# Kernel optimization log

Measured on AMD Instinct MI355X. Metric: run time of the kernel, lower is better.

## Reference

```python
import jax, jax.numpy as jnp
import numpy as np

B, T, C = 8, 2048, 1024      # batch, timesteps, input_dim
G, E = 2, 320                # groups_dim, entries_dim
EMB = 512                    # emb_dim
D = EMB // G                 # true_emb_dim per group


def setup_inputs() -> dict:
    key = jax.random.key(0)
    k1, k2, k3 = jax.random.split(key, 3)
    X = jax.random.normal(k1, (B, T, C), dtype=jnp.float32)
    # nn.Linear(input_dim, G*E): weight (out,in) ~ N(0,1), bias zeros
    W = jax.random.normal(k2, (G * E, C), dtype=jnp.float32)
    b = jnp.zeros((G * E,), dtype=jnp.float32)
    # codebook Parameter(1, G*E, D) ~ U[0,1); stored squeezed as (G*E, D)
    codebook = jax.random.uniform(k3, (G * E, D), dtype=jnp.float32)
    return {"X": X, "W": W, "b": b, "codebook": codebook}


def reference(X, W, b, codebook):
    # Eval-mode forward of VectorQuantization (time_first=True).
    nB, nT, _ = X.shape
    logits = jnp.einsum("btc,kc->btk", X, W) + b           # (B, T, G*E)
    # Faithful to source: view (B,T,G*E) as (B*G, T*E) and argmax over last dim
    flat = logits.reshape(nB * G, nT * E)                   # (B*G, T*E)
    k = jnp.argmax(flat, axis=-1)                           # (B*G,)
    hard = jax.nn.one_hot(k, nT * E, dtype=logits.dtype)    # (B*G, T*E)
    q = hard.reshape(nB * nT, G, E)                         # (B*T, G, E)
    # (one-hot * codebook).sum over entries == per-group gather
    cb = codebook.reshape(G, E, D)                          # (G, E, D)
    out = jnp.einsum("nge,ged->ngd", q, cb)                 # (B*T, G, D)
    return out.reshape(nB, nT, G * D)                       # (B, T, emb_dim)
```

## Files before the change

### kernel.cpp

```cpp
#include <hip/hip_runtime.h>
#include <stdint.h>

#define CC    1024
#define EE    320
#define KN    640
#define DD    256
#define MTOT  16384
#define NBLK  640
#define OUT4  2097152
#define MARGIN 12.0f

typedef __attribute__((ext_vector_type(8))) short short8;
typedef __attribute__((ext_vector_type(4))) float f32x4;
typedef __attribute__((ext_vector_type(2))) long longx2;

__device__ __forceinline__ unsigned int f32_orderable(float x) {
    unsigned int b = __float_as_uint(x);
    return (b & 0x80000000u) ? ~b : (b | 0x80000000u);
}

__global__ void init_slots_kernel(unsigned long long* __restrict__ slots) {
    if (threadIdx.x < 17) slots[threadIdx.x] = 0ull;
}

__global__ __launch_bounds__(256)
void convert_kernel(const float* __restrict__ X, const float* __restrict__ W,
                    unsigned char* __restrict__ A2F8, unsigned char* __restrict__ B2F8,
                    unsigned long long* __restrict__ slots, float* __restrict__ out) {
    const int bid = blockIdx.x;
    const int tid = threadIdx.x;
    {
        f32x4 z = {0.f, 0.f, 0.f, 0.f};
#pragma unroll
        for (int j = 0; j < 2; j++) {
            int zidx = bid * 512 + j * 256 + tid;
            if (zidx < OUT4) __builtin_nontemporal_store(z, (f32x4*)out + zidx);
        }
    }
    const int lane = tid & 63;
    const float* src;
    unsigned char* dst;
    int punit;
    if (bid < 4096) {
        punit = bid * 4 + (tid >> 6);
        src = X; dst = A2F8;
    } else {
        if (bid == 4096 && tid < 17) slots[tid] = 0ull;
        punit = (bid - 4096) * 4 + (tid >> 6);
        src = W; dst = B2F8;
    }
    int rt = punit >> 4, kc2 = punit & 15;
    int row = rt * 16 + (lane & 15);
    int col = kc2 * 64 + ((lane >> 4) << 3);
    const float* p = src + (size_t)row * CC + col;
    float4 v0 = *(const float4*)p;
    float4 v1 = *(const float4*)(p + 4);
    float4 v2 = *(const float4*)(p + 32);
    float4 v3 = *(const float4*)(p + 36);
    int d0 = __builtin_amdgcn_cvt_pk_fp8_f32(v0.x, v0.y, 0, false);
    d0     = __builtin_amdgcn_cvt_pk_fp8_f32(v0.z, v0.w, d0, true);
    int d1 = __builtin_amdgcn_cvt_pk_fp8_f32(v1.x, v1.y, 0, false);
    d1     = __builtin_amdgcn_cvt_pk_fp8_f32(v1.z, v1.w, d1, true);
    int d2 = __builtin_amdgcn_cvt_pk_fp8_f32(v2.x, v2.y, 0, false);
    d2     = __builtin_amdgcn_cvt_pk_fp8_f32(v2.z, v2.w, d2, true);
    int d3 = __builtin_amdgcn_cvt_pk_fp8_f32(v3.x, v3.y, 0, false);
    d3     = __builtin_amdgcn_cvt_pk_fp8_f32(v3.z, v3.w, d3, true);
    *(int4*)(dst + (size_t)punit * 1024 + lane * 16) = make_int4(d0, d1, d2, d3);
}

__global__ __launch_bounds__(256, 3)
void gemm_argmax_mfma(const unsigned char* __restrict__ A2F8,
                      const unsigned char* __restrict__ B2F8,
                      const float* __restrict__ X,
                      const float* __restrict__ W,
                      const float* __restrict__ bias,
                      const float* __restrict__ codebook,
                      float* __restrict__ out,
                      unsigned long long* __restrict__ slots,
                      unsigned int* __restrict__ counter) {
    __shared__ float redf[4];
    __shared__ int cnt_s;
    __shared__ int cand_s[128];
    __shared__ unsigned int done_s;
    __shared__ unsigned long long s16[16];

    const int tid  = threadIdx.x;
    const int lane = tid & 63;
    const int wave = tid >> 6;

    const int l   = blockIdx.x;
    const int xcd = l & 7;
    const int w   = l >> 3;
    const int mt  = xcd * 16 + w / 5;
    const int nt  = w % 5;
    const int m0 = mt * 128;
    const int n0 = nt * 128;

    const int wm = (wave >> 1) * 64;
    const int wn = (wave & 1) * 64;

    const unsigned char* Ap[4];
    const unsigned char* Bp[4];
#pragma unroll
    for (int t = 0; t < 4; t++) {
        Ap[t] = A2F8 + ((size_t)(((m0 + wm) >> 4) + t) * 16) * 1024 + lane * 16;
        Bp[t] = B2F8 + ((size_t)(((n0 + wn) >> 4) + t) * 16) * 1024 + lane * 16;
    }

    f32x4 acc[4][4] = {};
    longx2 a0[4], b0[4], a1[4], b1[4];

#pragma unroll
    for (int t = 0; t < 4; t++) {
        a0[t] = *(const longx2*)(Ap[t]);
        b0[t] = *(const longx2*)(Bp[t]);
        Ap[t] += 1024; Bp[t] += 1024;
    }

#define STEP(CURA, CURB, NXTA, NXTB, IT)                                         \
    {                                                                            \
        if ((IT) < 15) {                                                         \
            _Pragma("unroll")                                                    \
            for (int t = 0; t < 4; t++) {                                        \
                NXTA[t] = *(const longx2*)(Ap[t]);                               \
                NXTB[t] = *(const longx2*)(Bp[t]);                               \
                Ap[t] += 1024; Bp[t] += 1024;                                    \
            }                                                                    \
        }                                                                        \
        _Pragma("unroll")                                                        \
        for (int h = 0; h < 2; h++)                                              \
            _Pragma("unroll")                                                    \
            for (int ti = 0; ti < 4; ti++)                                       \
                _Pragma("unroll")                                                \
                for (int tj = 0; tj < 4; tj++)                                   \
                    acc[ti][tj] = __builtin_amdgcn_mfma_f32_16x16x32_fp8_fp8(    \
                        CURA[ti][h], CURB[tj][h], acc[ti][tj], 0, 0, 0);         \
    }

    for (int it2 = 0; it2 < 8; it2++) {
        STEP(a0, b0, a1, b1, it2 * 2)
        STEP(a1, b1, a0, b0, it2 * 2 + 1)
    }
#undef STEP

    float bias4[4];
#pragma unroll
    for (int tj = 0; tj < 4; tj++) bias4[tj] = bias[n0 + wn + tj * 16 + (lane & 15)];

    float vmax = -3.0e38f;
#pragma unroll
    for (int ti = 0; ti < 4; ti++)
#pragma unroll
        for (int tj = 0; tj < 4; tj++)
#pragma unroll
            for (int r = 0; r < 4; r++)
                vmax = fmaxf(vmax, acc[ti][tj][r] + bias4[tj]);
#pragma unroll
    for (int off = 32; off > 0; off >>= 1)
        vmax = fmaxf(vmax, __shfl_down(vmax, off, 64));
    if (lane == 0) redf[wave] = vmax;
    if (tid == 0) cnt_s = 0;
    __syncthreads();
    float bm = fmaxf(fmaxf(redf[0], redf[1]), fmaxf(redf[2], redf[3]));
    float thresh = bm - MARGIN;

#pragma unroll
    for (int ti = 0; ti < 4; ti++) {
#pragma unroll
        for (int r = 0; r < 4; r++) {
            int m = m0 + wm + ti * 16 + (lane >> 4) * 4 + r;
#pragma unroll
            for (int tj = 0; tj < 4; tj++) {
                float v = acc[ti][tj][r] + bias4[tj];
                if (v >= thresh) {
                    int n = n0 + wn + tj * 16 + (lane & 15);
                    int idx = atomicAdd(&cnt_s, 1);
                    if (idx < 128) cand_s[idx] = (m << 10) | n;
                }
            }
        }
    }
    __syncthreads();
    int cnt = cnt_s < 128 ? cnt_s : 128;

    for (int i = 0; i < cnt; i++) {
        int mc = cand_s[i] >> 10;
        int nc = cand_s[i] & 1023;
        float4 xv = *(const float4*)(X + (size_t)mc * CC + tid * 4);
        float4 wv = *(const float4*)(W + (size_t)nc * CC + tid * 4);
        float p = xv.x * wv.x + xv.y * wv.y + xv.z * wv.z + xv.w * wv.w;
#pragma unroll
        for (int off = 32; off > 0; off >>= 1) p += __shfl_down(p, off, 64);
        if (lane == 0) redf[wave] = p;
        __syncthreads();
        if (tid == 0) {
            float tot = redf[0] + redf[1] + redf[2] + redf[3] + bias[nc];
            unsigned int c = (unsigned int)((mc & 1023) * KN + nc);
            unsigned long long pk =
                ((unsigned long long)f32_orderable(tot) << 32) |
                (unsigned long long)(~c);
            atomicMax(slots + (mc >> 10), pk);
        }
        __syncthreads();
    }

    if (tid == 0) {
        __threadfence();
        done_s = atomicAdd(counter, 1u);
    }
    __syncthreads();

    if (done_s == NBLK - 1) {
        if (tid < 16) s16[tid] = atomicAdd(slots + tid, 0ull);
        __syncthreads();
        int rr  = tid >> 4;
        int seg = tid & 15;
        unsigned long long p = s16[rr];
        unsigned int c = ~(unsigned int)(p & 0xFFFFFFFFull);
        int tl = (int)(c / KN);
        int kg = (int)(c % KN);
        int b  = rr >> 1, h = rr & 1;
        int nstar = b * 2048 + h * 1024 + tl;
        int g = kg / EE;
        const float4* src = (const float4*)(codebook + (size_t)kg * DD) + seg * 4;
        float4* dst = (float4*)(out + (size_t)nstar * 512 + (size_t)g * DD) + seg * 4;
#pragma unroll
        for (int j = 0; j < 4; j++) dst[j] = src[j];
    }
}

__global__ __launch_bounds__(256)
void zs_kernel(const unsigned long long* __restrict__ slots,
               const float* __restrict__ codebook,
               float4* __restrict__ out4) {
    int i4 = blockIdx.x * 256 + threadIdx.x;
    int n  = i4 >> 7;
    int c4 = i4 & 127;
    int b  = n >> 11;
    int h  = (n >> 10) & 1;
    unsigned long long p = slots[b * 2 + h];
    unsigned int c = ~(unsigned int)(p & 0xFFFFFFFFull);
    int tl = (int)(c / KN);
    int kg = (int)(c % KN);
    int nstar = b * 2048 + h * 1024 + tl;
    int g = kg / EE;
    float4 v = make_float4(0.f, 0.f, 0.f, 0.f);
    if (n == nstar && (c4 >> 6) == g)
        v = ((const float4*)codebook)[kg * 64 + (c4 & 63)];
    out4[i4] = v;
}

#define BM 128
#define BN 64
#define BK 32
#define LDA (BM + 4)
#define LDB (BN + 4)

__global__ __launch_bounds__(128)
void gemm_argmax_f32(const float* __restrict__ X, const float* __restrict__ W,
                     const float* __restrict__ bias,
                     unsigned long long* __restrict__ slots) {
    __shared__ float Asf[BK][LDA];
    __shared__ float Bsf[BK][LDB];
    const int tid = threadIdx.x;
    const int m0 = blockIdx.y * BM;
    const int n0 = blockIdx.x * BN;
    const int tx = tid & 7, ty = tid >> 3;
    float acc[8][8];
#pragma unroll
    for (int i = 0; i < 8; i++)
#pragma unroll
        for (int j = 0; j < 8; j++) acc[i][j] = 0.0f;
    const int lm = tid >> 3, lk = (tid & 7) * 4;
    const float* Xb = X + (size_t)m0 * CC;
    const float* Wb = W + (size_t)n0 * CC;
    for (int k0 = 0; k0 < CC; k0 += BK) {
#pragma unroll
        for (int r = 0; r < 8; r++) {
            int m = r * 16 + lm;
            float4 v = *(const float4*)(Xb + (size_t)m * CC + k0 + lk);
            Asf[lk + 0][m] = v.x; Asf[lk + 1][m] = v.y; Asf[lk + 2][m] = v.z; Asf[lk + 3][m] = v.w;
        }
#pragma unroll
        for (int r = 0; r < 4; r++) {
            int m = r * 16 + lm;
            float4 v = *(const float4*)(Wb + (size_t)m * CC + k0 + lk);
            Bsf[lk + 0][m] = v.x; Bsf[lk + 1][m] = v.y; Bsf[lk + 2][m] = v.z; Bsf[lk + 3][m] = v.w;
        }
        __syncthreads();
#pragma unroll
        for (int kk = 0; kk < BK; kk++) {
            float4 A0 = *(const float4*)&Asf[kk][ty * 8];
            float4 A1 = *(const float4*)&Asf[kk][ty * 8 + 4];
            float4 B0 = *(const float4*)&Bsf[kk][tx * 8];
            float4 B1 = *(const float4*)&Bsf[kk][tx * 8 + 4];
            float a[8] = {A0.x, A0.y, A0.z, A0.w, A1.x, A1.y, A1.z, A1.w};
            float b[8] = {B0.x, B0.y, B0.z, B0.w, B1.x, B1.y, B1.z, B1.w};
#pragma unroll
            for (int i = 0; i < 8; i++)
#pragma unroll
                for (int j = 0; j < 8; j++) acc[i][j] = fmaf(a[i], b[j], acc[i][j]);
        }
        __syncthreads();
    }
    unsigned long long best = 0ull;
#pragma unroll
    for (int i = 0; i < 8; i++) {
        int mg = m0 + ty * 8 + i;
        int tl = mg & 1023;
#pragma unroll
        for (int j = 0; j < 8; j++) {
            int kg = n0 + tx * 8 + j;
            float v = acc[i][j] + bias[kg];
            unsigned int c = (unsigned int)(tl * KN + kg);
            unsigned long long p = ((unsigned long long)f32_orderable(v) << 32) |
                                   (unsigned long long)(~c);
            if (p > best) best = p;
        }
    }
#pragma unroll
    for (int off = 32; off > 0; off >>= 1) {
        unsigned long long o = __shfl_down(best, off, 64);
        if (o > best) best = o;
    }
    __shared__ unsigned long long red2[2];
    if ((tid & 63) == 0) red2[tid >> 6] = best;
    __syncthreads();
    if (tid == 0) {
        unsigned long long b0 = red2[0], b1 = red2[1];
        atomicMax(slots + (m0 >> 10), b0 > b1 ? b0 : b1);
    }
}

extern "C" void kernel_launch(void* const* d_in, const int* in_sizes, int n_in,
                              void* d_out, int out_size, void* d_ws, size_t ws_size,
                              hipStream_t stream) {
    const float* X        = (const float*)d_in[0];
    const float* W        = (const float*)d_in[1];
    const float* bias     = (const float*)d_in[2];
    const float* codebook = (const float*)d_in[3];
    float* out = (float*)d_out;

    unsigned long long* slots = (unsigned long long*)d_ws;
    unsigned int* counter = (unsigned int*)(slots + 16);
    const size_t A_off   = 256;
    const size_t A_bytes = (size_t)MTOT * CC;
    const size_t B_off   = A_off + A_bytes;
    const size_t B_bytes = (size_t)KN * CC;
    const size_t need = B_off + B_bytes;

    if (ws_size >= need) {
        unsigned char* A2F8 = (unsigned char*)d_ws + A_off;
        unsigned char* B2F8 = (unsigned char*)d_ws + B_off;
        hipLaunchKernelGGL(convert_kernel, dim3(4096 + 160), dim3(256), 0, stream,
                           X, W, A2F8, B2F8, slots, out);
        hipLaunchKernelGGL(gemm_argmax_mfma, dim3(NBLK), dim3(256), 0, stream,
                           A2F8, B2F8, X, W, bias, codebook, out, slots, counter);
    } else {
        hipLaunchKernelGGL(init_slots_kernel, dim3(1), dim3(64), 0, stream, slots);
        hipLaunchKernelGGL(gemm_argmax_f32, dim3(KN / BN, MTOT / BM), dim3(128), 0, stream,
                           X, W, bias, slots);
        hipLaunchKernelGGL(zs_kernel, dim3(OUT4 / 256), dim3(256), 0, stream,
                           slots, codebook, (float4*)out);
    }
}
```

Before: 153.2 us.

## Stage FP8 GEMM tiles through LDS with async global_load_lds double buffering

Replaces per-wave direct global loads of A/B fragments (each wave reloading tiles shared with sibling waves) with block-cooperative global_load_lds copies into a double-buffered 32KB LDS region, then reads fragments from LDS for the MFMA loop. This is meant to remove redundant global/L2 traffic, since each A and B tile was previously fetched by two waves. It adds a __syncthreads per K-step and 32KB of LDS per block, which may cut occupancy below the requested 3 blocks per CU. Correctness relies on global_load_lds completing before the barrier without explicit vmcnt waits.

```diff
diff --git a/kernel.cpp b/kernel.cpp
--- a/kernel.cpp
+++ b/kernel.cpp
@@ -78,6 +78,7 @@
                       float* __restrict__ out,
                       unsigned long long* __restrict__ slots,
                       unsigned int* __restrict__ counter) {
+    __shared__ __align__(16) unsigned char lds[32768];
     __shared__ float redf[4];
     __shared__ int cnt_s;
     __shared__ int cand_s[128];
@@ -99,49 +100,63 @@
     const int wm = (wave >> 1) * 64;
     const int wn = (wave & 1) * 64;
 
-    const unsigned char* Ap[4];
-    const unsigned char* Bp[4];
-#pragma unroll
-    for (int t = 0; t < 4; t++) {
-        Ap[t] = A2F8 + ((size_t)(((m0 + wm) >> 4) + t) * 16) * 1024 + lane * 16;
-        Bp[t] = B2F8 + ((size_t)(((n0 + wn) >> 4) + t) * 16) * 1024 + lane * 16;
-    }
+    const unsigned char* sA0 = A2F8 + (size_t)(((m0 >> 4) + wave)     ) * 16384 + lane * 16;
+    const unsigned char* sA1 = A2F8 + (size_t)(((m0 >> 4) + wave + 4) ) * 16384 + lane * 16;
+    const unsigned char* sB0 = B2F8 + (size_t)(((n0 >> 4) + wave)     ) * 16384 + lane * 16;
+    const unsigned char* sB1 = B2F8 + (size_t)(((n0 >> 4) + wave + 4) ) * 16384 + lane * 16;
+    const int dA0 = wave * 1024;
+    const int dA1 = (wave + 4) * 1024;
+    const int dB0 = 8192 + wave * 1024;
+    const int dB1 = 8192 + (wave + 4) * 1024;
 
     f32x4 acc[4][4] = {};
-    longx2 a0[4], b0[4], a1[4], b1[4];
-
-#pragma unroll
-    for (int t = 0; t < 4; t++) {
-        a0[t] = *(const longx2*)(Ap[t]);
-        b0[t] = *(const longx2*)(Bp[t]);
-        Ap[t] += 1024; Bp[t] += 1024;
-    }
-
-#define STEP(CURA, CURB, NXTA, NXTB, IT)                                         \
-    {                                                                            \
-        if ((IT) < 15) {                                                         \
-            _Pragma("unroll")                                                    \
-            for (int t = 0; t < 4; t++) {                                        \
-                NXTA[t] = *(const longx2*)(Ap[t]);                               \
-                NXTB[t] = *(const longx2*)(Bp[t]);                               \
-                Ap[t] += 1024; Bp[t] += 1024;                                    \
-            }                                                                    \
-        }                                                                        \
-        _Pragma("unroll")                                                        \
-        for (int h = 0; h < 2; h++)                                              \
-            _Pragma("unroll")                                                    \
-            for (int ti = 0; ti < 4; ti++)                                       \
-                _Pragma("unroll")                                                \
-                for (int tj = 0; tj < 4; tj++)                                   \
-                    acc[ti][tj] = __builtin_amdgcn_mfma_f32_16x16x32_fp8_fp8(    \
-                        CURA[ti][h], CURB[tj][h], acc[ti][tj], 0, 0, 0);         \
-    }
-
-    for (int it2 = 0; it2 < 8; it2++) {
-        STEP(a0, b0, a1, b1, it2 * 2)
-        STEP(a1, b1, a0, b0, it2 * 2 + 1)
-    }
-#undef STEP
+
+#define STAGE(BUF, T)                                                                     \
+    {                                                                                     \
+        __builtin_amdgcn_global_load_lds(                                                 \
+            (const __attribute__((address_space(1))) void*)(sA0 + (size_t)(T) * 1024),    \
+            (__attribute__((address_space(3))) void*)(lds + (BUF) + dA0), 16, 0, 0);      \
+        __builtin_amdgcn_global_load_lds(                                                 \
+            (const __attribute__((address_space(1))) void*)(sA1 + (size_t)(T) * 1024),    \
+            (__attribute__((address_space(3))) void*)(lds + (BUF) + dA1), 16, 0, 0);      \
+        __builtin_amdgcn_global_load_lds(                                                 \
+            (const __attribute__((address_space(1))) void*)(sB0 + (size_t)(T) * 1024),    \
+            (__attribute__((address_space(3))) void*)(lds + (BUF) + dB0), 16, 0, 0);      \
+        __builtin_amdgcn_global_load_lds(                                                 \
+            (const __attribute__((address_space(1))) void*)(sB1 + (size_t)(T) * 1024),    \
+            (__attribute__((address_space(3))) void*)(lds + (BUF) + dB1), 16, 0, 0);      \
+    }
+
+#define COMPUTE(BUF)                                                                      \
+    {                                                                                     \
+        longx2 af[4], bfr[4];                                                             \
+        _Pragma("unroll")                                                                 \
+        for (int t = 0; t < 4; t++) {                                                     \
+            af[t]  = *(const longx2*)(lds + (BUF) + (((wm >> 4) + t) << 10) + lane * 16); \
+            bfr[t] = *(const longx2*)(lds + (BUF) + 8192 + (((wn >> 4) + t) << 10) + lane * 16); \
+        }                                                                                 \
+        _Pragma("unroll")                                                                 \
+        for (int h = 0; h < 2; h++)                                                       \
+            _Pragma("unroll")                                                             \
+            for (int ti = 0; ti < 4; ti++)                                                \
+                _Pragma("unroll")                                                         \
+                for (int tj = 0; tj < 4; tj++)                                            \
+                    acc[ti][tj] = __builtin_amdgcn_mfma_f32_16x16x32_fp8_fp8(             \
+                        af[ti][h], bfr[tj][h], acc[ti][tj], 0, 0, 0);                     \
+    }
+
+    STAGE(0, 0)
+    __syncthreads();
+
+    for (int it2 = 0; it2 < 7; it2++) {
+        STAGE(16384, 2 * it2 + 1) COMPUTE(0)     __syncthreads();
+        STAGE(0,     2 * it2 + 2) COMPUTE(16384) __syncthreads();
+    }
+    STAGE(16384, 15) COMPUTE(0) __syncthreads();
+    COMPUTE(16384)
+
+#undef STAGE
+#undef COMPUTE
 
     float bias4[4];
 #pragma unroll
```

Result: no change. 153.4 us (+0.1%).

## Fuse X fp8 conversion into GEMM and move output zeroing into GEMM

Applied to the files above, without the earlier changes.

Drops the separate pass that converted all of X to fp8 in a workspace. The GEMM now loads fp32 X directly and packs it to fp8 in registers right before the MFMAs. Output zeroing moves from the convert kernel into the GEMM prologue, so the prep kernel only converts W and clears the slots. This removes the write and re-read of a 16 MB fp8 copy of X. In exchange, the GEMM reads four times the A bytes, spends more conversion ALU, and each X tile is re-converted by the five N-tile blocks. Occupancy drops from 3 to 2 blocks per CU to make room for the extra registers.

```diff
diff --git a/kernel.cpp b/kernel.cpp
--- a/kernel.cpp
+++ b/kernel.cpp
@@ -8,11 +8,11 @@
 #define MTOT  16384
 #define NBLK  640
 #define OUT4  2097152
+#define ZPB   3277
 #define MARGIN 12.0f
 
 typedef __attribute__((ext_vector_type(8))) short short8;
 typedef __attribute__((ext_vector_type(4))) float f32x4;
-typedef __attribute__((ext_vector_type(2))) long longx2;
 
 __device__ __forceinline__ unsigned int f32_orderable(float x) {
     unsigned int b = __float_as_uint(x);
@@ -24,35 +24,15 @@
 }
 
 __global__ __launch_bounds__(256)
-void convert_kernel(const float* __restrict__ X, const float* __restrict__ W,
-                    unsigned char* __restrict__ A2F8, unsigned char* __restrict__ B2F8,
-                    unsigned long long* __restrict__ slots, float* __restrict__ out) {
-    const int bid = blockIdx.x;
-    const int tid = threadIdx.x;
-    {
-        f32x4 z = {0.f, 0.f, 0.f, 0.f};
-#pragma unroll
-        for (int j = 0; j < 2; j++) {
-            int zidx = bid * 512 + j * 256 + tid;
-            if (zidx < OUT4) __builtin_nontemporal_store(z, (f32x4*)out + zidx);
-        }
-    }
-    const int lane = tid & 63;
-    const float* src;
-    unsigned char* dst;
-    int punit;
-    if (bid < 4096) {
-        punit = bid * 4 + (tid >> 6);
-        src = X; dst = A2F8;
-    } else {
-        if (bid == 4096 && tid < 17) slots[tid] = 0ull;
-        punit = (bid - 4096) * 4 + (tid >> 6);
-        src = W; dst = B2F8;
-    }
+void prep_kernel(const float* __restrict__ W, unsigned char* __restrict__ B2F8,
+                 unsigned long long* __restrict__ slots) {
+    if (blockIdx.x == 0 && threadIdx.x < 17) slots[threadIdx.x] = 0ull;
+    const int lane = threadIdx.x & 63;
+    int punit = blockIdx.x * 4 + (threadIdx.x >> 6);
     int rt = punit >> 4, kc2 = punit & 15;
     int row = rt * 16 + (lane & 15);
     int col = kc2 * 64 + ((lane >> 4) << 3);
-    const float* p = src + (size_t)row * CC + col;
+    const float* p = W + (size_t)row * CC + col;
     float4 v0 = *(const float4*)p;
     float4 v1 = *(const float4*)(p + 4);
     float4 v2 = *(const float4*)(p + 32);
@@ -65,12 +45,11 @@
     d2     = __builtin_amdgcn_cvt_pk_fp8_f32(v2.z, v2.w, d2, true);
     int d3 = __builtin_amdgcn_cvt_pk_fp8_f32(v3.x, v3.y, 0, false);
     d3     = __builtin_amdgcn_cvt_pk_fp8_f32(v3.z, v3.w, d3, true);
-    *(int4*)(dst + (size_t)punit * 1024 + lane * 16) = make_int4(d0, d1, d2, d3);
-}
-
-__global__ __launch_bounds__(256, 3)
-void gemm_argmax_mfma(const unsigned char* __restrict__ A2F8,
-                      const unsigned char* __restrict__ B2F8,
+    *(int4*)(B2F8 + (size_t)punit * 1024 + lane * 16) = make_int4(d0, d1, d2, d3);
+}
+
+__global__ __launch_bounds__(256, 2)
+void gemm_argmax_mfma(const unsigned char* __restrict__ B2F8,
                       const float* __restrict__ X,
                       const float* __restrict__ W,
                       const float* __restrict__ bias,
@@ -99,49 +78,87 @@
     const int wm = (wave >> 1) * 64;
     const int wn = (wave & 1) * 64;
 
-    const unsigned char* Ap[4];
-    const unsigned char* Bp[4];
-#pragma unroll
-    for (int t = 0; t < 4; t++) {
-        Ap[t] = A2F8 + ((size_t)(((m0 + wm) >> 4) + t) * 16) * 1024 + lane * 16;
-        Bp[t] = B2F8 + ((size_t)(((n0 + wn) >> 4) + t) * 16) * 1024 + lane * 16;
-    }
+    const float* Ap[4];
+#pragma unroll
+    for (int f = 0; f < 4; f++)
+        Ap[f] = X + (size_t)(m0 + wm + f * 16 + (lane & 15)) * CC + ((lane >> 4) << 3);
+    const unsigned char* Bq[4];
+#pragma unroll
+    for (int f = 0; f < 4; f++)
+        Bq[f] = B2F8 + (size_t)(((n0 + wn) >> 4) + f) * 16384 + lane * 16;
 
     f32x4 acc[4][4] = {};
-    longx2 a0[4], b0[4], a1[4], b1[4];
-
-#pragma unroll
-    for (int t = 0; t < 4; t++) {
-        a0[t] = *(const longx2*)(Ap[t]);
-        b0[t] = *(const longx2*)(Bp[t]);
-        Ap[t] += 1024; Bp[t] += 1024;
-    }
-
-#define STEP(CURA, CURB, NXTA, NXTB, IT)                                         \
+    float4 a0[4][2], a1[4][2];
+    long long b0[4], b1[4];
+
+#define LOADA(BUF, IT)                                                           \
     {                                                                            \
-        if ((IT) < 15) {                                                         \
+        _Pragma("unroll")                                                        \
+        for (int f = 0; f < 4; f++) {                                            \
+            BUF[f][0] = *(const float4*)(Ap[f] + (IT) * 32);                     \
+            BUF[f][1] = *(const float4*)(Ap[f] + (IT) * 32 + 4);                 \
+        }                                                                        \
+    }
+#define LOADB_EVEN(BUF, PU)                                                      \
+    {                                                                            \
+        _Pragma("unroll")                                                        \
+        for (int f = 0; f < 4; f++)                                              \
+            BUF[f] = *(const long long*)(Bq[f] + (size_t)(PU) * 1024);           \
+    }
+#define LOADB_ODD(BUF, PU)                                                       \
+    {                                                                            \
+        _Pragma("unroll")                                                        \
+        for (int f = 0; f < 4; f++)                                              \
+            BUF[f] = *(const long long*)(Bq[f] + (size_t)(PU) * 1024 + 8);       \
+    }
+#define MFMAS(AB, BB)                                                            \
+    {                                                                            \
+        long long af[4];                                                         \
+        _Pragma("unroll")                                                        \
+        for (int f = 0; f < 4; f++) {                                            \
+            int lo = __builtin_amdgcn_cvt_pk_fp8_f32(AB[f][0].x, AB[f][0].y, 0, false); \
+            lo     = __builtin_amdgcn_cvt_pk_fp8_f32(AB[f][0].z, AB[f][0].w, lo, true); \
+            int hi = __builtin_amdgcn_cvt_pk_fp8_f32(AB[f][1].x, AB[f][1].y, 0, false); \
+            hi     = __builtin_amdgcn_cvt_pk_fp8_f32(AB[f][1].z, AB[f][1].w, hi, true); \
+            af[f] = ((long long)hi << 32) | (long long)(unsigned)lo;             \
+        }                                                                        \
+        _Pragma("unroll")                                                        \
+        for (int ti = 0; ti < 4; ti++)                                           \
             _Pragma("unroll")                                                    \
-            for (int t = 0; t < 4; t++) {                                        \
-                NXTA[t] = *(const longx2*)(Ap[t]);                               \
-                NXTB[t] = *(const longx2*)(Bp[t]);                               \
-                Ap[t] += 1024; Bp[t] += 1024;                                    \
-            }                                                                    \
-        }                                                                        \
-        _Pragma("unroll")                                                        \
-        for (int h = 0; h < 2; h++)                                              \
-            _Pragma("unroll")                                                    \
-            for (int ti = 0; ti < 4; ti++)                                       \
-                _Pragma("unroll")                                                \
-                for (int tj = 0; tj < 4; tj++)                                   \
-                    acc[ti][tj] = __builtin_amdgcn_mfma_f32_16x16x32_fp8_fp8(    \
-                        CURA[ti][h], CURB[tj][h], acc[ti][tj], 0, 0, 0);         \
-    }
-
-    for (int it2 = 0; it2 < 8; it2++) {
-        STEP(a0, b0, a1, b1, it2 * 2)
-        STEP(a1, b1, a0, b0, it2 * 2 + 1)
-    }
-#undef STEP
+            for (int tj = 0; tj < 4; tj++)                                       \
+                acc[ti][tj] = __builtin_amdgcn_mfma_f32_16x16x32_fp8_fp8(        \
+                    af[ti], BB[tj], acc[ti][tj], 0, 0, 0);                       \
+    }
+
+    LOADA(a0, 0)
+    LOADB_EVEN(b0, 0)
+    {
+        int base = l * ZPB;
+        f32x4 z = {0.f, 0.f, 0.f, 0.f};
+        for (int j = 0; j < 13; j++) {
+            int o = j * 256 + tid;
+            int idx = base + o;
+            if (o < ZPB && idx < OUT4)
+                __builtin_nontemporal_store(z, (f32x4*)out + idx);
+        }
+    }
+
+    for (int it2 = 0; it2 < 16; it2++) {
+        if (it2 < 16) {
+            LOADA(a1, 2 * it2 + 1)
+            LOADB_ODD(b1, it2)
+        }
+        MFMAS(a0, b0)
+        if (it2 < 15) {
+            LOADA(a0, 2 * it2 + 2)
+            LOADB_EVEN(b0, it2 + 1)
+        }
+        MFMAS(a1, b1)
+    }
+#undef LOADA
+#undef LOADB_EVEN
+#undef LOADB_ODD
+#undef MFMAS
 
     float bias4[4];
 #pragma unroll
@@ -343,19 +360,15 @@
 
     unsigned long long* slots = (unsigned long long*)d_ws;
     unsigned int* counter = (unsigned int*)(slots + 16);
-    const size_t A_off   = 256;
-    const size_t A_bytes = (size_t)MTOT * CC;
-    const size_t B_off   = A_off + A_bytes;
+    const size_t B_off   = 256;
     const size_t B_bytes = (size_t)KN * CC;
     const size_t need = B_off + B_bytes;
 
     if (ws_size >= need) {
-        unsigned char* A2F8 = (unsigned char*)d_ws + A_off;
         unsigned char* B2F8 = (unsigned char*)d_ws + B_off;
-        hipLaunchKernelGGL(convert_kernel, dim3(4096 + 160), dim3(256), 0, stream,
-                           X, W, A2F8, B2F8, slots, out);
+        hipLaunchKernelGGL(prep_kernel, dim3(160), dim3(256), 0, stream, W, B2F8, slots);
         hipLaunchKernelGGL(gemm_argmax_mfma, dim3(NBLK), dim3(256), 0, stream,
-                           A2F8, B2F8, X, W, bias, codebook, out, slots, counter);
+                           B2F8, X, W, bias, codebook, out, slots, counter);
     } else {
         hipLaunchKernelGGL(init_slots_kernel, dim3(1), dim3(64), 0, stream, slots);
         hipLaunchKernelGGL(gemm_argmax_f32, dim3(KN / BN, MTOT / BM), dim3(128), 0, stream,
```

New measurement: 220.4 us. 1.44x slower.
